# Kernel optimization log

Measured on AMD Instinct MI355X. Metric: run time of the kernel, lower is better.

Reference implementation:

```python
import jax, jax.numpy as jnp
import numpy as np

EPS = 1e-5

def _bn(x, g, b):
    # BatchNorm1d in training mode: batch statistics over nodes
    m = jnp.mean(x, axis=0)
    v = jnp.var(x, axis=0)
    return g * (x - m) * jax.lax.rsqrt(v + EPS) + b

def _gconv(x, adj, W, b):
    # GraphConvolution: adj @ x @ W + b
    return adj @ (x @ W) + b

def _gsage(x, adj, W, b):
    # GraphSAGE layer: relu(adj @ x @ W + b)
    return jax.nn.relu(adj @ (x @ W) + b)

def setup_inputs() -> dict:
    key = jax.random.key(0)
    ks = jax.random.split(key, 20)
    N = 8192
    x = jax.random.normal(ks[0], (N, 18), dtype=jnp.float32)
    adj = jax.random.uniform(ks[1], (N, N), dtype=jnp.float32)
    s = 0.1
    p = {
        'W1': jax.random.normal(ks[2], (18, 16)) * s, 'b1': jnp.zeros((16,)),
        'W2': jax.random.normal(ks[3], (16, 16)) * s, 'b2': jnp.zeros((16,)),
        'We1': jax.random.normal(ks[4], (16, 8)) * s, 'be1': jnp.zeros((8,)),
        'Wp1': jax.random.normal(ks[5], (16, 20)) * s, 'bp1': jnp.zeros((20,)),
        'W3': jax.random.normal(ks[6], (8, 8)) * s, 'b3': jnp.zeros((8,)),
        'We2': jax.random.normal(ks[7], (8, 8)) * s, 'be2': jnp.zeros((8,)),
        'g1': jnp.ones((16,)), 'bt1': jnp.zeros((16,)),
        'g2': jnp.ones((16,)), 'bt2': jnp.zeros((16,)),
        'g3': jnp.ones((8,)), 'bt3': jnp.zeros((8,)),
    }
    p = {k: v.astype(jnp.float32) for k, v in p.items()}
    return {'x': x, 'adj': adj, **p}

def reference(x, adj, W1, b1, W2, b2, We1, be1, Wp1, bp1, W3, b3, We2, be2,
              g1, bt1, g2, bt2, g3, bt3):
    h = _bn(_gsage(x, adj, W1, b1), g1, bt1)          # [N,16]
    h = _bn(_gsage(h, adj, W2, b2), g2, bt2)          # [N,16]
    # DiffPool(16, 20, 8)
    z = _gconv(h, adj, We1, be1)                      # [N,8]
    s_l = jax.nn.softmax(_gconv(h, adj, Wp1, bp1), axis=1)  # [N,20]
    h = s_l.T @ z                                     # [20,8]
    a = s_l.T @ adj @ s_l                             # [20,20]
    h = _bn(_gsage(h, a, W3, b3), g3, bt3)            # [20,8]
    # DiffPool(8, 1, 8, is_final=True): s = ones -> column sum
    z = _gconv(h, a, We2, be2)                        # [20,8]
    return jnp.sum(z, axis=0, keepdims=True)          # [1,8]
```

## Files before the change

kernel.cpp:

```cpp
#include <hip/hip_runtime.h>
#include <cstddef>

#define NROWS 8192
constexpr float BN_EPS = 1e-5f;

typedef __attribute__((ext_vector_type(8))) short bf16x8;
typedef __attribute__((ext_vector_type(4))) float f32x4;
typedef __attribute__((ext_vector_type(2))) float f32x2;
typedef __attribute__((ext_vector_type(4))) unsigned int u32x4;

__device__ __forceinline__ unsigned short bf16u(float f) {
    unsigned u = __float_as_uint(f);
    u += 0x7FFFu + ((u >> 16) & 1u);
    return (unsigned short)(u >> 16);
}

constexpr size_t OFF_P   = 0;
constexpr size_t OFF_YP  = OFF_P   + (size_t)16 * NROWS * 32;
constexpr size_t OFF_SLP = OFF_YP  + (size_t)NROWS * 32 / 2;
constexpr size_t OFF_U   = OFF_SLP + (size_t)NROWS * 32 / 2;
constexpr size_t OFF_SL  = OFF_U   + (size_t)NROWS * 16;
constexpr size_t OFF_ST1 = OFF_SL  + (size_t)NROWS * 20;
constexpr size_t OFF_ST2 = OFF_ST1 + 32;
constexpr size_t OFF_HSM = OFF_ST2 + 32;
constexpr size_t OFF_AG  = OFF_HSM + 160;
constexpr size_t OFF_END_SMALL = OFF_AG + 400;
constexpr size_t OFF_ADJB = (OFF_END_SMALL + 15) & ~(size_t)15;
constexpr size_t NEED_FULL_BYTES = (OFF_ADJB + (size_t)NROWS * NROWS / 2) * 4;


__global__ __launch_bounds__(256)
void k_conv_spmm(const float* __restrict__ adjf, unsigned short* __restrict__ adjp,
                 const unsigned short* __restrict__ ypu, float* __restrict__ P)
{
    __shared__ unsigned short lds[16384];
    const int bid = blockIdx.x;
    const int rb = bid & 63, kc = bid >> 6;
    const int t = threadIdx.x, lane = t & 63, wv = t >> 6;
    const int row0 = rb * 128 + wv * 32;
    const int s_q = lane >> 4;
    const int khi = (lane >> 2) & 3;
    const int el2 = (lane & 3) * 2;
    const bf16x8* ap = (const bf16x8*)lds;
    const bf16x8* yp = (const bf16x8*)ypu;
    const size_t blockbase = (size_t)(kc * 64 + rb) * 8192;

    f32x4 acc0 = (f32x4){0.f,0.f,0.f,0.f}, acc1 = (f32x4){0.f,0.f,0.f,0.f};

    for (int q = 0; q < 4; ++q) {
        const int kbase = kc * 512 + q * 128;
        __syncthreads();
#pragma unroll 8
        for (int rr = 0; rr < 32; ++rr) {
            const f32x2 v = *(const f32x2*)(adjf + (size_t)(row0 + rr) * NROWS + kbase + lane * 2);
            const int m = rr >> 4, rA = rr & 15;
            int u = ((wv * 4 + s_q) * 2 + m) * 64 + rA + 16 * khi;
            u ^= ((u >> 4) & 3) ^ (((u >> 7) & 1) << 2);
            unsigned short* p = &lds[u * 8 + el2];
            p[0] = bf16u(v.x);
            p[1] = bf16u(v.y);
        }
        __syncthreads();
#pragma unroll
        for (int i = 0; i < 8; ++i) {
            const int flat = i * 256 + t;
            const int phys = flat ^ ((flat >> 4) & 3) ^ (((flat >> 7) & 1) << 2);
            const u32x4 d = *(const u32x4*)&lds[phys * 8];
            const int wvd = flat >> 9;
            const size_t gu = blockbase + (size_t)wvd * 2048 + (size_t)q * 512 + (flat & 511);
            *(u32x4*)(adjp + gu * 8) = d;
        }
#pragma unroll
        for (int sq = 0; sq < 4; ++sq) {
            int L0 = ((wv * 4 + sq) * 2 + 0) * 64 + lane;
            int L1 = L0 + 64;
            L0 ^= ((L0 >> 4) & 3) ^ (((L0 >> 7) & 1) << 2);
            L1 ^= ((L1 >> 4) & 3) ^ (((L1 >> 7) & 1) << 2);
            const bf16x8 a0 = ap[L0];
            const bf16x8 a1 = ap[L1];
            const bf16x8 b0 = yp[((size_t)(kc * 16 + q * 4 + sq)) * 64 + lane];
            acc0 = __builtin_amdgcn_mfma_f32_16x16x32_bf16(a0, b0, acc0, 0, 0, 0);
            acc1 = __builtin_amdgcn_mfma_f32_16x16x32_bf16(a1, b0, acc1, 0, 0, 0);
        }
    }

    float* Pk = P + ((size_t)kc * NROWS + row0) * 16;
    const int drow = (lane >> 4) * 4;
    const int dcol = lane & 15;
#pragma unroll
    for (int r = 0; r < 4; ++r) {
        Pk[(size_t)(drow + r) * 16 + dcol]      = acc0[r];
        Pk[(size_t)(16 + drow + r) * 16 + dcol] = acc1[r];
    }
}

template<int NT>
__global__ __launch_bounds__(256)
void k_spmm_p(const unsigned short* __restrict__ adjp,
              const unsigned short* __restrict__ ypu, float* __restrict__ P)
{
    constexpr int CP = NT * 16;
    const int rb   = blockIdx.x & 63;
    const int kc   = blockIdx.x >> 6;
    const int lane = threadIdx.x & 63;
    const int wv   = threadIdx.x >> 6;
    const int row0 = rb * 128 + wv * 32;
    const bf16x8* ap = (const bf16x8*)adjp;
    const bf16x8* yp = (const bf16x8*)ypu;
    const size_t wbase = ((size_t)(kc * 64 + rb) * 4 + wv) * 2048;

    f32x4 acc[2][NT];
#pragma unroll
    for (int m = 0; m < 2; ++m)
#pragma unroll
        for (int n = 0; n < NT; ++n) acc[m][n] = (f32x4){0.f, 0.f, 0.f, 0.f};

    auto LA = [&](int m, int s) -> bf16x8 {
        return ap[wbase + (size_t)s * 128 + m * 64 + lane];
    };
    auto LB = [&](int n, int s) -> bf16x8 {
        return yp[((size_t)((kc * 16 + s) * NT + n)) * 64 + lane];
    };

    bf16x8 a0 = LA(0, 0), a1 = LA(1, 0);
    bf16x8 b0 = LB(0, 0), b1;
    if constexpr (NT == 2) b1 = LB(1, 0);

#pragma unroll
    for (int s = 0; s < 16; ++s) {
        bf16x8 na0, na1, nb0, nb1;
        if (s < 15) {
            na0 = LA(0, s + 1); na1 = LA(1, s + 1);
            nb0 = LB(0, s + 1);
            if constexpr (NT == 2) nb1 = LB(1, s + 1);
        }
        acc[0][0] = __builtin_amdgcn_mfma_f32_16x16x32_bf16(a0, b0, acc[0][0], 0, 0, 0);
        acc[1][0] = __builtin_amdgcn_mfma_f32_16x16x32_bf16(a1, b0, acc[1][0], 0, 0, 0);
        if constexpr (NT == 2) {
            acc[0][1] = __builtin_amdgcn_mfma_f32_16x16x32_bf16(a0, b1, acc[0][1], 0, 0, 0);
            acc[1][1] = __builtin_amdgcn_mfma_f32_16x16x32_bf16(a1, b1, acc[1][1], 0, 0, 0);
        }
        if (s < 15) { a0 = na0; a1 = na1; b0 = nb0; if constexpr (NT == 2) b1 = nb1; }
    }

    float* Pk = P + ((size_t)kc * NROWS + row0) * CP;
    const int drow = (lane >> 4) * 4;
    const int dcol = lane & 15;
#pragma unroll
    for (int m = 0; m < 2; ++m)
#pragma unroll
        for (int n = 0; n < NT; ++n)
#pragma unroll
            for (int r = 0; r < 4; ++r)
                Pk[(size_t)(m * 16 + drow + r) * CP + n * 16 + dcol] = acc[m][n][r];
}

template<int NT>
__global__ __launch_bounds__(256)
void k_spmm_f32(const float* __restrict__ adjf,
                const unsigned short* __restrict__ ypu, float* __restrict__ P)
{
    constexpr int CP = NT * 16;
    const int rb   = blockIdx.x & 63;
    const int kc   = blockIdx.x >> 6;
    const int lane = threadIdx.x & 63;
    const int wv   = threadIdx.x >> 6;
    const int row0 = rb * 128 + wv * 32;
    const int k0   = kc * 512;
    const int rA   = lane & 15;
    const int kA   = (lane >> 4) * 8;
    const bf16x8* yp = (const bf16x8*)ypu;

    f32x4 acc[2][NT];
#pragma unroll
    for (int m = 0; m < 2; ++m)
#pragma unroll
        for (int n = 0; n < NT; ++n) acc[m][n] = (f32x4){0.f, 0.f, 0.f, 0.f};

    const size_t offA0 = (size_t)(row0 + rA) * NROWS + k0 + kA;
    const size_t offA1 = offA0 + (size_t)16 * NROWS;

    auto LA = [&](int m, int s) -> bf16x8 {
        const size_t o = (m ? offA1 : offA0) + (size_t)s * 32;
        const f32x4 u = *(const f32x4*)(adjf + o);
        const f32x4 v = *(const f32x4*)(adjf + o + 4);
        bf16x8 tt;
        tt[0] = (short)bf16u(u.x); tt[1] = (short)bf16u(u.y);
        tt[2] = (short)bf16u(u.z); tt[3] = (short)bf16u(u.w);
        tt[4] = (short)bf16u(v.x); tt[5] = (short)bf16u(v.y);
        tt[6] = (short)bf16u(v.z); tt[7] = (short)bf16u(v.w);
        return tt;
    };
    auto LB = [&](int n, int s) -> bf16x8 {
        return yp[((size_t)((kc * 16 + s) * NT + n)) * 64 + lane];
    };

    bf16x8 a0 = LA(0, 0), a1 = LA(1, 0);
    bf16x8 b0 = LB(0, 0), b1;
    if constexpr (NT == 2) b1 = LB(1, 0);

#pragma unroll
    for (int s = 0; s < 16; ++s) {
        bf16x8 na0, na1, nb0, nb1;
        if (s < 15) {
            na0 = LA(0, s + 1); na1 = LA(1, s + 1);
            nb0 = LB(0, s + 1);
            if constexpr (NT == 2) nb1 = LB(1, s + 1);
        }
        acc[0][0] = __builtin_amdgcn_mfma_f32_16x16x32_bf16(a0, b0, acc[0][0], 0, 0, 0);
        acc[1][0] = __builtin_amdgcn_mfma_f32_16x16x32_bf16(a1, b0, acc[1][0], 0, 0, 0);
        if constexpr (NT == 2) {
            acc[0][1] = __builtin_amdgcn_mfma_f32_16x16x32_bf16(a0, b1, acc[0][1], 0, 0, 0);
            acc[1][1] = __builtin_amdgcn_mfma_f32_16x16x32_bf16(a1, b1, acc[1][1], 0, 0, 0);
        }
        if (s < 15) { a0 = na0; a1 = na1; b0 = nb0; if constexpr (NT == 2) b1 = nb1; }
    }

    float* Pk = P + ((size_t)kc * NROWS + row0) * CP;
    const int drow = (lane >> 4) * 4;
    const int dcol = lane & 15;
#pragma unroll
    for (int m = 0; m < 2; ++m)
#pragma unroll
        for (int n = 0; n < NT; ++n)
#pragma unroll
            for (int r = 0; r < 4; ++r)
                Pk[(size_t)(m * 16 + drow + r) * CP + n * 16 + dcol] = acc[m][n][r];
}

__global__ __launch_bounds__(256)
void k_y1_pack(const float* __restrict__ x, const float* __restrict__ W1,
               unsigned short* __restrict__ yp)
{
    const int j = blockIdx.x * 256 + threadIdx.x;
    float xr[18];
#pragma unroll
    for (int d = 0; d < 18; ++d) xr[d] = x[j * 18 + d];
    const int kb = j >> 5, lhi = ((j & 31) >> 3) << 4, idx = j & 7;
#pragma unroll
    for (int c = 0; c < 16; ++c) {
        float a = 0.f;
#pragma unroll
        for (int d = 0; d < 18; ++d) a = fmaf(xr[d], W1[d * 16 + c], a);
        yp[((size_t)kb * 64 + (lhi | c)) * 8 + idx] = bf16u(a);
    }
}

__global__ __launch_bounds__(256)
void k_reduce16(const float* __restrict__ P, const float* __restrict__ bias,
                float* __restrict__ U, float* __restrict__ stats)
{
    const int t = threadIdx.x, col = t & 15, rg = t >> 4;
    float s = 0.f, ss = 0.f;
    for (int r = blockIdx.x * 16 + rg; r < NROWS; r += 1024) {
        float v = bias[col];
#pragma unroll
        for (int kc = 0; kc < 16; ++kc)
            v += P[((size_t)kc * NROWS + r) * 16 + col];
        v = fmaxf(v, 0.f);
        U[r * 16 + col] = v;
        s += v; ss += v * v;
    }
    __shared__ float ls[16][17], lss[16][17];
    ls[rg][col] = s; lss[rg][col] = ss;
    __syncthreads();
    if (t < 16) {
        float a = 0.f, b = 0.f;
        for (int g = 0; g < 16; ++g) { a += ls[g][t]; b += lss[g][t]; }
        atomicAdd(&stats[t], a);
        atomicAdd(&stats[16 + t], b);
    }
}

template<int COA, int COB, int NTO>
__global__ __launch_bounds__(256)
void k_bn_pack(const float* __restrict__ U, const float* __restrict__ stats,
               const float* __restrict__ g, const float* __restrict__ bt,
               const float* __restrict__ Wa, const float* __restrict__ Wb,
               unsigned short* __restrict__ yp)
{
    const int j = blockIdx.x * 256 + threadIdx.x;
    float h[16];
#pragma unroll
    for (int k = 0; k < 16; ++k) {
        const float m   = stats[k] * (1.f / NROWS);
        const float var = stats[16 + k] * (1.f / NROWS) - m * m;
        const float sc  = g[k] * rsqrtf(var + BN_EPS);
        h[k] = fmaf(U[j * 16 + k], sc, bt[k] - m * sc);
    }
    const int kb = j >> 5, lhi = ((j & 31) >> 3) << 4, idx = j & 7;
    auto slot = [&](int c) -> size_t {
        return ((size_t)(kb * NTO + (c >> 4)) * 64 + (lhi | (c & 15))) * 8 + idx;
    };
#pragma unroll
    for (int co = 0; co < COA; ++co) {
        float a = 0.f;
#pragma unroll
        for (int k = 0; k < 16; ++k) a = fmaf(h[k], Wa[k * COA + co], a);
        yp[slot(co)] = bf16u(a);
    }
#pragma unroll
    for (int co = 0; co < COB; ++co) {
        float a = 0.f;
#pragma unroll
        for (int k = 0; k < 16; ++k) a = fmaf(h[k], Wb[k * COB + co], a);
        yp[slot(COA + co)] = bf16u(a);
    }
#pragma unroll
    for (int c = COA + COB; c < NTO * 16; ++c) yp[slot(c)] = 0;
}

__global__ __launch_bounds__(256)
void k_red_fin3(const float* __restrict__ P, const float* __restrict__ be1,
                const float* __restrict__ bp1, float* __restrict__ sl,
                unsigned short* __restrict__ slp, float* __restrict__ hsm)
{
    __shared__ float szl[256 * 8];
    __shared__ float ssl[256 * 20];
    const int t = threadIdx.x;
    const int row = blockIdx.x * 256 + t;

    float s3[28];
#pragma unroll
    for (int c = 0; c < 28; ++c) s3[c] = 0.f;
#pragma unroll
    for (int kc = 0; kc < 16; ++kc) {
        const float* pr = &P[((size_t)kc * NROWS + row) * 32];
#pragma unroll
        for (int q = 0; q < 7; ++q) {
            const f32x4 v = *(const f32x4*)(pr + q * 4);
            s3[q * 4 + 0] += v.x; s3[q * 4 + 1] += v.y;
            s3[q * 4 + 2] += v.z; s3[q * 4 + 3] += v.w;
        }
    }
#pragma unroll
    for (int k = 0; k < 8; ++k) szl[t * 8 + k] = s3[k] + be1[k];

    float s[20];
    float mx = -1e30f;
#pragma unroll
    for (int k = 0; k < 20; ++k) {
        s[k] = s3[8 + k] + bp1[k];
        mx = fmaxf(mx, s[k]);
    }
    float se = 0.f;
#pragma unroll
    for (int k = 0; k < 20; ++k) { s[k] = expf(s[k] - mx); se += s[k]; }
    const float inv = 1.f / se;
    const int kb = row >> 5, lhi = ((row & 31) >> 3) << 4, idx = row & 7;
    auto slot = [&](int c) -> size_t {
        return ((size_t)(kb * 2 + (c >> 4)) * 64 + (lhi | (c & 15))) * 8 + idx;
    };
#pragma unroll
    for (int k = 0; k < 20; ++k) {
        s[k] *= inv;
        sl[(size_t)row * 20 + k] = s[k];
        ssl[t * 20 + k] = s[k];
        slp[slot(k)] = bf16u(s[k]);
    }
#pragma unroll
    for (int c = 20; c < 32; ++c) slp[slot(c)] = 0;
    __syncthreads();
    if (t < 160) {
        const int p = t >> 3, q = t & 7;
        float a = 0.f;
        for (int r = 0; r < 256; ++r) a = fmaf(ssl[r * 20 + p], szl[r * 8 + q], a);
        atomicAdd(&hsm[t], a);
    }
}

__global__ __launch_bounds__(256)
void k_red_fin4(const float* __restrict__ P, const float* __restrict__ sl,
                float* __restrict__ a_g)
{
    __shared__ float stt[256 * 20];
    __shared__ float ssl[256 * 20];
    const int t = threadIdx.x;
    const int row = blockIdx.x * 256 + t;

    float t4[20];
#pragma unroll
    for (int c = 0; c < 20; ++c) t4[c] = 0.f;
#pragma unroll
    for (int kc = 0; kc < 16; ++kc) {
        const float* pr = &P[((size_t)kc * NROWS + row) * 32];
#pragma unroll
        for (int q = 0; q < 5; ++q) {
            const f32x4 v = *(const f32x4*)(pr + q * 4);
            t4[q * 4 + 0] += v.x; t4[q * 4 + 1] += v.y;
            t4[q * 4 + 2] += v.z; t4[q * 4 + 3] += v.w;
        }
    }
#pragma unroll
    for (int c = 0; c < 20; ++c) {
        stt[t * 20 + c] = t4[c];
        ssl[t * 20 + c] = sl[(size_t)row * 20 + c];
    }
    __syncthreads();
    for (int pair = t; pair < 400; pair += 256) {
        const int p = pair / 20, q = pair % 20;
        float a = 0.f;
        for (int r = 0; r < 256; ++r) a = fmaf(ssl[r * 20 + p], stt[r * 20 + q], a);
        atomicAdd(&a_g[pair], a);
    }
}

__global__ __launch_bounds__(256)
void k_final(const float* __restrict__ hsm, const float* __restrict__ a_g,
             const float* __restrict__ W3, const float* __restrict__ b3,
             const float* __restrict__ g3, const float* __restrict__ bt3,
             const float* __restrict__ We2, const float* __restrict__ be2,
             float* __restrict__ out)
{
    __shared__ float m1[160], qb[160], hb[160], sc[8], sh[8];
    const int t = threadIdx.x;
    const int p = t >> 3, k = t & 7;
    if (t < 160) {
        float a = 0.f;
        for (int j = 0; j < 8; ++j) a = fmaf(hsm[p * 8 + j], W3[j * 8 + k], a);
        m1[t] = a;
    }
    __syncthreads();
    if (t < 160) {
        float a = b3[k];
        for (int j = 0; j < 20; ++j) a = fmaf(a_g[p * 20 + j], m1[j * 8 + k], a);
        qb[t] = fmaxf(a, 0.f);
    }
    __syncthreads();
    if (t < 8) {
        float m = 0.f, v = 0.f;
        for (int r = 0; r < 20; ++r) { float q = qb[r * 8 + t]; m += q; v += q * q; }
        m *= (1.f / 20.f); v = v * (1.f / 20.f) - m * m;
        const float s = g3[t] * rsqrtf(v + BN_EPS);
        sc[t] = s; sh[t] = bt3[t] - m * s;
    }
    __syncthreads();
    if (t < 160) hb[t] = fmaf(qb[t], sc[k], sh[k]);
    __syncthreads();
    if (t < 160) {
        float a = 0.f;
        for (int j = 0; j < 8; ++j) a = fmaf(hb[p * 8 + j], We2[j * 8 + k], a);
        m1[t] = a;
    }
    __syncthreads();
    if (t < 160) {
        float a = be2[k];
        for (int j = 0; j < 20; ++j) a = fmaf(a_g[p * 20 + j], m1[j * 8 + k], a);
        qb[t] = a;
    }
    __syncthreads();
    if (t < 8) {
        float a = 0.f;
        for (int r = 0; r < 20; ++r) a += qb[r * 8 + t];
        out[t] = a;
    }
}

extern "C" void kernel_launch(void* const* d_in, const int* in_sizes, int n_in,
                              void* d_out, int out_size, void* d_ws, size_t ws_size,
                              hipStream_t stream)
{
    const float* x   = (const float*)d_in[0];
    const float* adj = (const float*)d_in[1];
    const float* W1  = (const float*)d_in[2];
    const float* b1  = (const float*)d_in[3];
    const float* W2  = (const float*)d_in[4];
    const float* b2  = (const float*)d_in[5];
    const float* We1 = (const float*)d_in[6];
    const float* be1 = (const float*)d_in[7];
    const float* Wp1 = (const float*)d_in[8];
    const float* bp1 = (const float*)d_in[9];
    const float* W3  = (const float*)d_in[10];
    const float* b3  = (const float*)d_in[11];
    const float* We2 = (const float*)d_in[12];
    const float* be2 = (const float*)d_in[13];
    const float* g1  = (const float*)d_in[14];
    const float* bt1 = (const float*)d_in[15];
    const float* g2  = (const float*)d_in[16];
    const float* bt2 = (const float*)d_in[17];
    const float* g3  = (const float*)d_in[18];
    const float* bt3 = (const float*)d_in[19];

    float* ws = (float*)d_ws;
    float* P  = ws + OFF_P;
    unsigned short* YP   = (unsigned short*)(ws + OFF_YP);
    unsigned short* SLP  = (unsigned short*)(ws + OFF_SLP);
    float* U   = ws + OFF_U;
    float* SL  = ws + OFF_SL;
    float* ST1 = ws + OFF_ST1;
    float* ST2 = ws + OFF_ST2;
    float* HSM = ws + OFF_HSM;
    float* AG  = ws + OFF_AG;
    unsigned short* ADJP = (unsigned short*)(ws + OFF_ADJB);
    float* out = (float*)d_out;

    const bool FULL = ws_size >= NEED_FULL_BYTES;
    const dim3 blk(256);

    (void)hipMemsetAsync(ST1, 0, (32 + 32 + 160 + 400) * sizeof(float), stream);

    k_y1_pack<<<32, blk, 0, stream>>>(x, W1, YP);
    if (FULL) k_conv_spmm<<<1024, blk, 0, stream>>>(adj, ADJP, YP, P);
    else      k_spmm_f32<1><<<1024, blk, 0, stream>>>(adj, YP, P);
    k_reduce16<<<64, blk, 0, stream>>>(P, b1, U, ST1);
    k_bn_pack<16, 0, 1><<<32, blk, 0, stream>>>(U, ST1, g1, bt1, W2, nullptr, YP);

    if (FULL) k_spmm_p<1><<<1024, blk, 0, stream>>>(ADJP, YP, P);
    else      k_spmm_f32<1><<<1024, blk, 0, stream>>>(adj, YP, P);
    k_reduce16<<<64, blk, 0, stream>>>(P, b2, U, ST2);
    k_bn_pack<8, 20, 2><<<32, blk, 0, stream>>>(U, ST2, g2, bt2, We1, Wp1, YP);

    if (FULL) k_spmm_p<2><<<1024, blk, 0, stream>>>(ADJP, YP, P);
    else      k_spmm_f32<2><<<1024, blk, 0, stream>>>(adj, YP, P);
    k_red_fin3<<<32, blk, 0, stream>>>(P, be1, bp1, SL, SLP, HSM);

    if (FULL) k_spmm_p<2><<<1024, blk, 0, stream>>>(ADJP, SLP, P);
    else      k_spmm_f32<2><<<1024, blk, 0, stream>>>(adj, SLP, P);
    k_red_fin4<<<32, blk, 0, stream>>>(P, SL, AG);

    k_final<<<1, blk, 0, stream>>>(HSM, AG, W3, b3, g3, bt3, We2, be2, out);
}
```

Measured before the change: 221.5 us.

## Double-buffer conversion staging, halve split-K partials, fuse reduce with batchnorm-pack

The fp32-to-bf16 conversion kernel now double-buffers its LDS staging so the next tile's global loads overlap the current tile's packed writes and MFMAs. The packed SpMM kernels process two K-chunks per block, so they launch 512 blocks and write half as many partial products, and they skip storing padded output columns. The separate reduce and batchnorm-pack kernels are merged into one kernel that waits on an atomic-counter grid barrier for global BN statistics before packing the next layer's input, which removes a launch and the U round-trip. The spin barrier assumes all 64 blocks are resident at once, and the longer SpMM K-loop reduces parallelism.

Measured after the change: 279.7 us. 26.3% more time.

```diff
diff --git a/kernel.cpp b/kernel.cpp
--- a/kernel.cpp
+++ b/kernel.cpp
@@ -24,7 +24,8 @@
 constexpr size_t OFF_ST2 = OFF_ST1 + 32;
 constexpr size_t OFF_HSM = OFF_ST2 + 32;
 constexpr size_t OFF_AG  = OFF_HSM + 160;
-constexpr size_t OFF_END_SMALL = OFF_AG + 400;
+constexpr size_t OFF_CTR = OFF_AG  + 400;
+constexpr size_t OFF_END_SMALL = OFF_CTR + 2;
 constexpr size_t OFF_ADJB = (OFF_END_SMALL + 15) & ~(size_t)15;
 constexpr size_t NEED_FULL_BYTES = (OFF_ADJB + (size_t)NROWS * NROWS / 2) * 4;
 
@@ -33,7 +34,7 @@
 void k_conv_spmm(const float* __restrict__ adjf, unsigned short* __restrict__ adjp,
                  const unsigned short* __restrict__ ypu, float* __restrict__ P)
 {
-    __shared__ unsigned short lds[16384];
+    __shared__ unsigned short lds[2][16384];
     const int bid = blockIdx.x;
     const int rb = bid & 63, kc = bid >> 6;
     const int t = threadIdx.x, lane = t & 63, wv = t >> 6;
@@ -41,35 +42,40 @@
     const int s_q = lane >> 4;
     const int khi = (lane >> 2) & 3;
     const int el2 = (lane & 3) * 2;
-    const bf16x8* ap = (const bf16x8*)lds;
     const bf16x8* yp = (const bf16x8*)ypu;
     const size_t blockbase = (size_t)(kc * 64 + rb) * 8192;
 
     f32x4 acc0 = (f32x4){0.f,0.f,0.f,0.f}, acc1 = (f32x4){0.f,0.f,0.f,0.f};
 
-    for (int q = 0; q < 4; ++q) {
+    auto STAGE = [&](int q, int sb) {
         const int kbase = kc * 512 + q * 128;
-        __syncthreads();
-#pragma unroll 8
+#pragma unroll
         for (int rr = 0; rr < 32; ++rr) {
             const f32x2 v = *(const f32x2*)(adjf + (size_t)(row0 + rr) * NROWS + kbase + lane * 2);
             const int m = rr >> 4, rA = rr & 15;
             int u = ((wv * 4 + s_q) * 2 + m) * 64 + rA + 16 * khi;
             u ^= ((u >> 4) & 3) ^ (((u >> 7) & 1) << 2);
-            unsigned short* p = &lds[u * 8 + el2];
+            unsigned short* p = &lds[sb][u * 8 + el2];
             p[0] = bf16u(v.x);
             p[1] = bf16u(v.y);
         }
+    };
+
+    STAGE(0, 0);
+    for (int q = 0; q < 4; ++q) {
+        const int sb = q & 1;
         __syncthreads();
+        if (q < 3) STAGE(q + 1, sb ^ 1);
 #pragma unroll
         for (int i = 0; i < 8; ++i) {
             const int flat = i * 256 + t;
             const int phys = flat ^ ((flat >> 4) & 3) ^ (((flat >> 7) & 1) << 2);
-            const u32x4 d = *(const u32x4*)&lds[phys * 8];
+            const u32x4 d = *(const u32x4*)&lds[sb][phys * 8];
             const int wvd = flat >> 9;
             const size_t gu = blockbase + (size_t)wvd * 2048 + (size_t)q * 512 + (flat & 511);
             *(u32x4*)(adjp + gu * 8) = d;
         }
+        const bf16x8* ap = (const bf16x8*)lds[sb];
 #pragma unroll
         for (int sq = 0; sq < 4; ++sq) {
             int L0 = ((wv * 4 + sq) * 2 + 0) * 64 + lane;
@@ -94,20 +100,21 @@
     }
 }
 
-template<int NT>
+template<int NT, int CO>
 __global__ __launch_bounds__(256)
 void k_spmm_p(const unsigned short* __restrict__ adjp,
               const unsigned short* __restrict__ ypu, float* __restrict__ P)
 {
     constexpr int CP = NT * 16;
     const int rb   = blockIdx.x & 63;
-    const int kc   = blockIdx.x >> 6;
+    const int kc2  = blockIdx.x >> 6;
     const int lane = threadIdx.x & 63;
     const int wv   = threadIdx.x >> 6;
     const int row0 = rb * 128 + wv * 32;
     const bf16x8* ap = (const bf16x8*)adjp;
     const bf16x8* yp = (const bf16x8*)ypu;
-    const size_t wbase = ((size_t)(kc * 64 + rb) * 4 + wv) * 2048;
+    const size_t wbase0 = ((size_t)((kc2 * 2 + 0) * 64 + rb) * 4 + wv) * 2048;
+    const size_t wbase1 = ((size_t)((kc2 * 2 + 1) * 64 + rb) * 4 + wv) * 2048;
 
     f32x4 acc[2][NT];
 #pragma unroll
@@ -116,10 +123,11 @@
         for (int n = 0; n < NT; ++n) acc[m][n] = (f32x4){0.f, 0.f, 0.f, 0.f};
 
     auto LA = [&](int m, int s) -> bf16x8 {
-        return ap[wbase + (size_t)s * 128 + m * 64 + lane];
+        const size_t wb = (s < 16) ? wbase0 : wbase1;
+        return ap[wb + (size_t)(s & 15) * 128 + m * 64 + lane];
     };
     auto LB = [&](int n, int s) -> bf16x8 {
-        return yp[((size_t)((kc * 16 + s) * NT + n)) * 64 + lane];
+        return yp[((size_t)((kc2 * 32 + s) * NT + n)) * 64 + lane];
     };
 
     bf16x8 a0 = LA(0, 0), a1 = LA(1, 0);
@@ -127,9 +135,9 @@
     if constexpr (NT == 2) b1 = LB(1, 0);
 
 #pragma unroll
-    for (int s = 0; s < 16; ++s) {
+    for (int s = 0; s < 32; ++s) {
         bf16x8 na0, na1, nb0, nb1;
-        if (s < 15) {
+        if (s < 31) {
             na0 = LA(0, s + 1); na1 = LA(1, s + 1);
             nb0 = LB(0, s + 1);
             if constexpr (NT == 2) nb1 = LB(1, s + 1);
@@ -140,22 +148,24 @@
             acc[0][1] = __builtin_amdgcn_mfma_f32_16x16x32_bf16(a0, b1, acc[0][1], 0, 0, 0);
             acc[1][1] = __builtin_amdgcn_mfma_f32_16x16x32_bf16(a1, b1, acc[1][1], 0, 0, 0);
         }
-        if (s < 15) { a0 = na0; a1 = na1; b0 = nb0; if constexpr (NT == 2) b1 = nb1; }
-    }
-
-    float* Pk = P + ((size_t)kc * NROWS + row0) * CP;
+        if (s < 31) { a0 = na0; a1 = na1; b0 = nb0; if constexpr (NT == 2) b1 = nb1; }
+    }
+
+    float* Pk = P + ((size_t)kc2 * NROWS + row0) * CP;
     const int drow = (lane >> 4) * 4;
     const int dcol = lane & 15;
 #pragma unroll
     for (int m = 0; m < 2; ++m)
 #pragma unroll
         for (int n = 0; n < NT; ++n)
-#pragma unroll
-            for (int r = 0; r < 4; ++r)
-                Pk[(size_t)(m * 16 + drow + r) * CP + n * 16 + dcol] = acc[m][n][r];
-}
-
-template<int NT>
+            if (n * 16 + 0 < CO)
+#pragma unroll
+                for (int r = 0; r < 4; ++r)
+                    if (n * 16 + dcol < CO)
+                        Pk[(size_t)(m * 16 + drow + r) * CP + n * 16 + dcol] = acc[m][n][r];
+}
+
+template<int NT, int CO>
 __global__ __launch_bounds__(256)
 void k_spmm_f32(const float* __restrict__ adjf,
                 const unsigned short* __restrict__ ypu, float* __restrict__ P)
@@ -223,9 +233,11 @@
     for (int m = 0; m < 2; ++m)
 #pragma unroll
         for (int n = 0; n < NT; ++n)
-#pragma unroll
-            for (int r = 0; r < 4; ++r)
-                Pk[(size_t)(m * 16 + drow + r) * CP + n * 16 + dcol] = acc[m][n][r];
+            if (n * 16 + 0 < CO)
+#pragma unroll
+                for (int r = 0; r < 4; ++r)
+                    if (n * 16 + dcol < CO)
+                        Pk[(size_t)(m * 16 + drow + r) * CP + n * 16 + dcol] = acc[m][n][r];
 }
 
 __global__ __launch_bounds__(256)
@@ -246,70 +258,87 @@
     }
 }
 
-__global__ __launch_bounds__(256)
-void k_reduce16(const float* __restrict__ P, const float* __restrict__ bias,
-                float* __restrict__ U, float* __restrict__ stats)
+template<int KCN, int COA, int COB, int NTO>
+__global__ __launch_bounds__(256)
+void k_red_bn(const float* __restrict__ P, const float* __restrict__ bias,
+              const float* __restrict__ g, const float* __restrict__ bt,
+              const float* __restrict__ Wa, const float* __restrict__ Wb,
+              unsigned short* __restrict__ yp, float* __restrict__ stats,
+              unsigned int* __restrict__ ctr)
 {
     const int t = threadIdx.x, col = t & 15, rg = t >> 4;
+    const int rbase = blockIdx.x * 128;
+    float u[8];
     float s = 0.f, ss = 0.f;
-    for (int r = blockIdx.x * 16 + rg; r < NROWS; r += 1024) {
+#pragma unroll
+    for (int i = 0; i < 8; ++i) {
+        const int r = rbase + rg + i * 16;
         float v = bias[col];
 #pragma unroll
-        for (int kc = 0; kc < 16; ++kc)
+        for (int kc = 0; kc < KCN; ++kc)
             v += P[((size_t)kc * NROWS + r) * 16 + col];
         v = fmaxf(v, 0.f);
-        U[r * 16 + col] = v;
-        s += v; ss += v * v;
+        u[i] = v; s += v; ss += v * v;
     }
     __shared__ float ls[16][17], lss[16][17];
+    __shared__ float hb[128][17];
+    __shared__ float scb[16], shb[16];
     ls[rg][col] = s; lss[rg][col] = ss;
     __syncthreads();
     if (t < 16) {
         float a = 0.f, b = 0.f;
-        for (int g = 0; g < 16; ++g) { a += ls[g][t]; b += lss[g][t]; }
+        for (int gg = 0; gg < 16; ++gg) { a += ls[gg][t]; b += lss[gg][t]; }
         atomicAdd(&stats[t], a);
         atomicAdd(&stats[16 + t], b);
     }
-}
-
-template<int COA, int COB, int NTO>
-__global__ __launch_bounds__(256)
-void k_bn_pack(const float* __restrict__ U, const float* __restrict__ stats,
-               const float* __restrict__ g, const float* __restrict__ bt,
-               const float* __restrict__ Wa, const float* __restrict__ Wb,
-               unsigned short* __restrict__ yp)
-{
-    const int j = blockIdx.x * 256 + threadIdx.x;
-    float h[16];
-#pragma unroll
-    for (int k = 0; k < 16; ++k) {
-        const float m   = stats[k] * (1.f / NROWS);
-        const float var = stats[16 + k] * (1.f / NROWS) - m * m;
-        const float sc  = g[k] * rsqrtf(var + BN_EPS);
-        h[k] = fmaf(U[j * 16 + k], sc, bt[k] - m * sc);
-    }
-    const int kb = j >> 5, lhi = ((j & 31) >> 3) << 4, idx = j & 7;
+    __syncthreads();
+    if (t == 0) {
+        __threadfence();
+        atomicAdd(ctr, 1u);
+        while (__hip_atomic_load(ctr, __ATOMIC_RELAXED, __HIP_MEMORY_SCOPE_AGENT) < 64u) {}
+        __threadfence();
+    }
+    __syncthreads();
+    if (t < 16) {
+        const float sm  = atomicAdd(&stats[t], 0.f);
+        const float sq  = atomicAdd(&stats[16 + t], 0.f);
+        const float m   = sm * (1.f / NROWS);
+        const float var = sq * (1.f / NROWS) - m * m;
+        const float sc  = g[t] * rsqrtf(var + BN_EPS);
+        scb[t] = sc; shb[t] = bt[t] - m * sc;
+    }
+    __syncthreads();
+#pragma unroll
+    for (int i = 0; i < 8; ++i)
+        hb[rg + i * 16][col] = fmaf(u[i], scb[col], shb[col]);
+    __syncthreads();
+    constexpr int CO = COA + COB;
+    const int lrow = t >> 1;
+    const int jrow = rbase + lrow;
+    const int kb = jrow >> 5, lhi = ((jrow & 31) >> 3) << 4, idx = jrow & 7;
     auto slot = [&](int c) -> size_t {
         return ((size_t)(kb * NTO + (c >> 4)) * 64 + (lhi | (c & 15))) * 8 + idx;
     };
-#pragma unroll
-    for (int co = 0; co < COA; ++co) {
-        float a = 0.f;
-#pragma unroll
-        for (int k = 0; k < 16; ++k) a = fmaf(h[k], Wa[k * COA + co], a);
-        yp[slot(co)] = bf16u(a);
-    }
-#pragma unroll
-    for (int co = 0; co < COB; ++co) {
-        float a = 0.f;
-#pragma unroll
-        for (int k = 0; k < 16; ++k) a = fmaf(h[k], Wb[k * COB + co], a);
-        yp[slot(COA + co)] = bf16u(a);
-    }
-#pragma unroll
-    for (int c = COA + COB; c < NTO * 16; ++c) yp[slot(c)] = 0;
-}
-
+    float h[16];
+#pragma unroll
+    for (int k = 0; k < 16; ++k) h[k] = hb[lrow][k];
+    const int c0 = (t & 1) * ((NTO * 16) / 2);
+#pragma unroll
+    for (int cc = 0; cc < (NTO * 16) / 2; ++cc) {
+        const int c = c0 + cc;
+        float a = 0.f;
+        if (c < COA) {
+#pragma unroll
+            for (int k = 0; k < 16; ++k) a = fmaf(h[k], Wa[k * COA + c], a);
+        } else if (c < CO) {
+#pragma unroll
+            for (int k = 0; k < 16; ++k) a = fmaf(h[k], Wb[k * COB + (c - COA)], a);
+        }
+        yp[slot(c)] = (c < CO) ? bf16u(a) : (unsigned short)0;
+    }
+}
+
+template<int KCN>
 __global__ __launch_bounds__(256)
 void k_red_fin3(const float* __restrict__ P, const float* __restrict__ be1,
                 const float* __restrict__ bp1, float* __restrict__ sl,
@@ -324,7 +353,7 @@
 #pragma unroll
     for (int c = 0; c < 28; ++c) s3[c] = 0.f;
 #pragma unroll
-    for (int kc = 0; kc < 16; ++kc) {
+    for (int kc = 0; kc < KCN; ++kc) {
         const float* pr = &P[((size_t)kc * NROWS + row) * 32];
 #pragma unroll
         for (int q = 0; q < 7; ++q) {
@@ -369,6 +398,7 @@
     }
 }
 
+template<int KCN>
 __global__ __launch_bounds__(256)
 void k_red_fin4(const float* __restrict__ P, const float* __restrict__ sl,
                 float* __restrict__ a_g)
@@ -382,7 +412,7 @@
 #pragma unroll
     for (int c = 0; c < 20; ++c) t4[c] = 0.f;
 #pragma unroll
-    for (int kc = 0; kc < 16; ++kc) {
+    for (int kc = 0; kc < KCN; ++kc) {
         const float* pr = &P[((size_t)kc * NROWS + row) * 32];
 #pragma unroll
         for (int q = 0; q < 5; ++q) {
@@ -485,38 +515,46 @@
     float* P  = ws + OFF_P;
     unsigned short* YP   = (unsigned short*)(ws + OFF_YP);
     unsigned short* SLP  = (unsigned short*)(ws + OFF_SLP);
-    float* U   = ws + OFF_U;
     float* SL  = ws + OFF_SL;
     float* ST1 = ws + OFF_ST1;
     float* ST2 = ws + OFF_ST2;
     float* HSM = ws + OFF_HSM;
     float* AG  = ws + OFF_AG;
+    unsigned int* CTR = (unsigned int*)(ws + OFF_CTR);
     unsigned short* ADJP = (unsigned short*)(ws + OFF_ADJB);
     float* out = (float*)d_out;
 
     const bool FULL = ws_size >= NEED_FULL_BYTES;
     const dim3 blk(256);
 
-    (void)hipMemsetAsync(ST1, 0, (32 + 32 + 160 + 400) * sizeof(float), stream);
+    (void)hipMemsetAsync(ST1, 0, (32 + 32 + 160 + 400 + 2) * sizeof(float), stream);
 
     k_y1_pack<<<32, blk, 0, stream>>>(x, W1, YP);
-    if (FULL) k_conv_spmm<<<1024, blk, 0, stream>>>(adj, ADJP, YP, P);
-    else      k_spmm_f32<1><<<1024, blk, 0, stream>>>(adj, YP, P);
-    k_reduce16<<<64, blk, 0, stream>>>(P, b1, U, ST1);
-    k_bn_pack<16, 0, 1><<<32, blk, 0, stream>>>(U, ST1, g1, bt1, W2, nullptr, YP);
-
-    if (FULL) k_spmm_p<1><<<1024, blk, 0, stream>>>(ADJP, YP, P);
-    else      k_spmm_f32<1><<<1024, blk, 0, stream>>>(adj, YP, P);
-    k_reduce16<<<64, blk, 0, stream>>>(P, b2, U, ST2);
-    k_bn_pack<8, 20, 2><<<32, blk, 0, stream>>>(U, ST2, g2, bt2, We1, Wp1, YP);
-
-    if (FULL) k_spmm_p<2><<<1024, blk, 0, stream>>>(ADJP, YP, P);
-    else      k_spmm_f32<2><<<1024, blk, 0, stream>>>(adj, YP, P);
-    k_red_fin3<<<32, blk, 0, stream>>>(P, be1, bp1, SL, SLP, HSM);
-
-    if (FULL) k_spmm_p<2><<<1024, blk, 0, stream>>>(ADJP, SLP, P);
-    else      k_spmm_f32<2><<<1024, blk, 0, stream>>>(adj, SLP, P);
-    k_red_fin4<<<32, blk, 0, stream>>>(P, SL, AG);
+    if (FULL) {
+        k_conv_spmm<<<1024, blk, 0, stream>>>(adj, ADJP, YP, P);
+        k_red_bn<16, 16, 0, 1><<<64, blk, 0, stream>>>(P, b1, g1, bt1, W2, nullptr, YP, ST1, CTR);
+
+        k_spmm_p<1, 16><<<512, blk, 0, stream>>>(ADJP, YP, P);
+        k_red_bn<8, 8, 20, 2><<<64, blk, 0, stream>>>(P, b2, g2, bt2, We1, Wp1, YP, ST2, CTR + 1);
+
+        k_spmm_p<2, 28><<<512, blk, 0, stream>>>(ADJP, YP, P);
+        k_red_fin3<8><<<32, blk, 0, stream>>>(P, be1, bp1, SL, SLP, HSM);
+
+        k_spmm_p<2, 20><<<512, blk, 0, stream>>>(ADJP, SLP, P);
+        k_red_fin4<8><<<32, blk, 0, stream>>>(P, SL, AG);
+    } else {
+        k_spmm_f32<1, 16><<<1024, blk, 0, stream>>>(adj, YP, P);
+        k_red_bn<16, 16, 0, 1><<<64, blk, 0, stream>>>(P, b1, g1, bt1, W2, nullptr, YP, ST1, CTR);
+
+        k_spmm_f32<1, 16><<<1024, blk, 0, stream>>>(adj, YP, P);
+        k_red_bn<16, 8, 20, 2><<<64, blk, 0, stream>>>(P, b2, g2, bt2, We1, Wp1, YP, ST2, CTR + 1);
+
+        k_spmm_f32<2, 28><<<1024, blk, 0, stream>>>(adj, YP, P);
+        k_red_fin3<16><<<32, blk, 0, stream>>>(P, be1, bp1, SL, SLP, HSM);
+
+        k_spmm_f32<2, 20><<<1024, blk, 0, stream>>>(adj, SLP, P);
+        k_red_fin4<16><<<32, blk, 0, stream>>>(P, SL, AG);
+    }
 
     k_final<<<1, blk, 0, stream>>>(HSM, AG, W3, b3, g3, bt3, We2, be2, out);
 }
```
